# Optimization experiments

Hardware: AMD Instinct MI355X
Metric: run time of the kernel (lower is better)

## Reference

```python
import jax, jax.numpy as jnp
import numpy as np

DIM = 1024
H = 16
HD = DIM // H
EPS_DENOM = 1e-6
EPS_LN = 1e-5


def setup_inputs() -> dict:
    key = jax.random.key(0)
    ks = jax.random.split(key, 8)
    B, N = 4, 4096
    s = 1.0 / np.sqrt(DIM)
    return {
        "x": jax.random.normal(ks[0], (B, N, DIM), dtype=jnp.float32),
        "Wq": jax.random.normal(ks[1], (DIM, DIM), dtype=jnp.float32) * s,
        "bq": jnp.zeros((DIM,), dtype=jnp.float32),
        "Wk": jax.random.normal(ks[2], (DIM, DIM), dtype=jnp.float32) * s,
        "bk": jnp.zeros((DIM,), dtype=jnp.float32),
        "Wv": jax.random.normal(ks[3], (DIM, DIM), dtype=jnp.float32) * s,
        "bv": jnp.zeros((DIM,), dtype=jnp.float32),
        "gamma": jnp.ones((DIM,), dtype=jnp.float32),
        "beta": jnp.zeros((DIM,), dtype=jnp.float32),
    }


def reference(x, Wq, bq, Wk, bk, Wv, bv, gamma, beta):
    B, N, C = x.shape
    # projections; torch Linear applies x @ W.T + b
    q = (x @ Wq.T + bq).reshape(B, N, H, HD)
    k = (x @ Wk.T + bk).reshape(B, N, H, HD)
    v = (x @ Wv.T + bv).reshape(B, N, H, HD)
    q = jax.nn.relu(q)
    k = jax.nn.relu(k)
    kv = jnp.einsum('bnhd,bnhp->bhdp', k, v)         # (B,H,D,D)
    k_sum = k.sum(axis=1)                             # (B,H,D)
    denom = jnp.einsum('bnhd,bhd->bnh', q, k_sum)
    denom = jnp.maximum(denom, EPS_DENOM)[..., None]  # (B,N,H,1)
    ctx = jnp.einsum('bnhd,bhdp->bnhp', q, kv)        # (B,N,H,D)
    out = (ctx / denom).reshape(B, N, C)
    y = out + x
    mu = y.mean(axis=-1, keepdims=True)
    var = y.var(axis=-1, keepdims=True)
    return (y - mu) / jnp.sqrt(var + EPS_LN) * gamma + beta
```

## Files before the change

kernel.cpp:

```cpp
#include <hip/hip_runtime.h>
#include <hip/hip_bf16.h>
#include <stdint.h>

#define DIM 1024
#define HEADS 16
#define HD 64
#define BB 4
#define NN 4096
#define NTOK (BB*NN)

typedef __bf16 bf16;
typedef __bf16 bf16x8 __attribute__((ext_vector_type(8)));
typedef float  f32x4  __attribute__((ext_vector_type(4)));
typedef unsigned short u16x8 __attribute__((ext_vector_type(8)));
typedef unsigned short u16x4 __attribute__((ext_vector_type(4)));

__device__ __forceinline__ float bf2f(unsigned short u) {
    union { unsigned int i; float f; } x; x.i = ((unsigned int)u) << 16; return x.f;
}

__device__ __forceinline__ u16x8 cvt8(f32x4 a, f32x4 b) {
    union { bf16 h[8]; u16x8 u; } r;
    #pragma unroll
    for (int i = 0; i < 4; ++i) { r.h[i] = (bf16)a[i]; r.h[4 + i] = (bf16)b[i]; }
    return r.u;
}

__device__ __forceinline__ u16x8 load8(const void* base, size_t elem, bool isbf) {
    if (isbf) return *(const u16x8*)((const unsigned short*)base + elem);
    const float* p = (const float*)base + elem;
    return cvt8(*(const f32x4*)p, *(const f32x4*)(p + 4));
}

__device__ __forceinline__ void async_copy16(const void* g, void* l) {
    __builtin_amdgcn_global_load_lds(
        (const __attribute__((address_space(1))) void*)g,
        (__attribute__((address_space(3))) void*)l,
        16, 0, 0);
}

__global__ __launch_bounds__(256) void convert_all(
    const void* __restrict__ X,
    const void* __restrict__ Wq, const void* __restrict__ Wk,
    const void* __restrict__ Wv, const uint32_t* __restrict__ det,
    u16x8* __restrict__ Xb, u16x8* __restrict__ Wb)
{
    const bool isbf = (*det == 0x3F803F80u);
    size_t e = ((size_t)blockIdx.x * 256 + threadIdx.x) * 8;
    if (e < 16777216ull) {
        Xb[e >> 3] = load8(X, e, isbf);
    } else {
        size_t r = e - 16777216ull;
        int w = (int)(r >> 20);
        const void* src = (w == 0) ? Wq : (w == 1) ? Wk : Wv;
        Wb[r >> 3] = load8(src, r & 1048575ull, isbf);
    }
}


#define MFMA_Q(Q) do {                                                        \
    _Pragma("unroll")                                                         \
    for (int kb_ = 0; kb_ < 2; ++kb_) {                                       \
        _Pragma("unroll")                                                     \
        for (int i_ = 0; i_ < 2; ++i_) {                                      \
            _Pragma("unroll")                                                 \
            for (int j_ = 0; j_ < 4; ++j_)                                    \
                acc[Q][i_][j_] = __builtin_amdgcn_mfma_f32_16x16x32_bf16(     \
                    afr[i_][kb_], bfrag[j_][kb_], acc[Q][i_][j_], 0, 0, 0);   \
        }                                                                     \
    }                                                                         \
} while (0)

#define PHASE(BUF, Q, DOB, STAGE_STMT, VM_STMT) do {                          \
    bf16x8 afr[2][2];                                                         \
    if (DOB) loadB(BUF);                                                      \
    loadA(BUF, Q, afr);                                                       \
    STAGE_STMT;                                                               \
    VM_STMT;                                                                  \
    __builtin_amdgcn_s_barrier();                                             \
    asm volatile("s_waitcnt lgkmcnt(0)" ::: "memory");                        \
    __builtin_amdgcn_s_setprio(1);                                            \
    MFMA_Q(Q);                                                                \
    __builtin_amdgcn_s_setprio(0);                                            \
    __builtin_amdgcn_s_barrier();                                             \
} while (0)

__global__ __launch_bounds__(512, 2) void qkv_gemm_8ph(
    const bf16* __restrict__ Xb, const bf16* __restrict__ Wb,
    const void* __restrict__ bq, const void* __restrict__ bk,
    const void* __restrict__ bv, const uint32_t* __restrict__ det,
    bf16* __restrict__ outQKV)
{
    extern __shared__ char lds[];

    const bool isbf = (*det == 0x3F803F80u);

    const int bid = blockIdx.x;
    const int xcd = bid & 7;
    const int idx = bid >> 3;
    const int mb  = xcd * 8 + (idx & 7);
    const int nb  = idx >> 3;
    const int m0  = mb * 256;
    const int n0  = nb * 256;
    const int z   = n0 >> 10;
    const int ncol0 = n0 & 1023;
    const void* bias = (z == 0) ? bq : (z == 1) ? bk : bv;
    bf16* out = outQKV + (size_t)z * (size_t)NTOK * DIM;

    const int tid  = threadIdx.x;
    const int wid  = tid >> 6;
    const int lane = tid & 63;
    const int lrow = lane & 15;
    const int lkq  = lane >> 4;
    const int wm   = wid >> 2;
    const int wn   = wid & 3;

    auto stageHT = [&](int kt, int which) {
        const int  buf = kt & 1;
        const bool isB = which >= 2;
        const int  gb  = (which & 1) * 8;
        char* base = lds + buf * 65536 + (isB ? 32768 : 0);
        const int k0 = kt * 64;
        #pragma unroll
        for (int t2 = 0; t2 < 2; ++t2) {
            int s   = wid * 2 + t2;
            int g   = gb + (s >> 1);
            int kb  = s & 1;
            int row = g * 16 + lrow;
            int kk  = k0 + kb * 32 + lkq * 8;
            const bf16* gp = isB ? (Wb + (size_t)(n0 + row) * DIM + kk)
                                 : (Xb + (size_t)(m0 + row) * DIM + kk);
            async_copy16(gp, base + (g * 2 + kb) * 1024);
        }
    };

    bf16x8 bfrag[4][2];
    auto loadB = [&](int buf) {
        char* bB = lds + buf * 65536 + 32768;
        #pragma unroll
        for (int j = 0; j < 4; ++j)
            #pragma unroll
            for (int kb = 0; kb < 2; ++kb)
                bfrag[j][kb] = *(const bf16x8*)(
                    bB + ((wn * 4 + j) * 2 + kb) * 1024 + lane * 16);
    };
    auto loadA = [&](int buf, int q, bf16x8 (&afr)[2][2]) {
        char* bA = lds + buf * 65536;
        #pragma unroll
        for (int i = 0; i < 2; ++i)
            #pragma unroll
            for (int kb = 0; kb < 2; ++kb)
                afr[i][kb] = *(const bf16x8*)(
                    bA + ((q * 4 + wm * 2 + i) * 2 + kb) * 1024 + lane * 16);
    };

    f32x4 acc[4][2][4];
    #pragma unroll
    for (int q = 0; q < 4; ++q)
        #pragma unroll
        for (int i = 0; i < 2; ++i)
            #pragma unroll
            for (int j = 0; j < 4; ++j)
                #pragma unroll
                for (int r = 0; r < 4; ++r) acc[q][i][j][r] = 0.f;

    stageHT(0, 0); stageHT(0, 1); stageHT(0, 2); stageHT(0, 3);
    stageHT(1, 0); stageHT(1, 1); stageHT(1, 2);
    asm volatile("s_waitcnt vmcnt(6)" ::: "memory");
    __builtin_amdgcn_s_barrier();

    for (int ip = 0; ip < 8; ++ip) {
        const int  t    = ip * 2;
        const bool more = (ip < 7);
        PHASE(0, 0, true,  { stageHT(t + 1, 3); },              {});
        PHASE(0, 1, false, { if (more) stageHT(t + 2, 2); },    {});
        PHASE(0, 2, false, { if (more) stageHT(t + 2, 0); },    {});
        PHASE(0, 3, false, { if (more) stageHT(t + 2, 3); },
              { if (more) { asm volatile("s_waitcnt vmcnt(6)" ::: "memory"); }
                else      { asm volatile("s_waitcnt vmcnt(0)" ::: "memory"); } });
        PHASE(1, 0, true,  { if (more) stageHT(t + 2, 1); },    {});
        PHASE(1, 1, false, { if (more) stageHT(t + 3, 2); },    {});
        PHASE(1, 2, false, { if (more) stageHT(t + 3, 0); },    {});
        PHASE(1, 3, false, { if (more) stageHT(t + 3, 1); },
              { if (more) { asm volatile("s_waitcnt vmcnt(6)" ::: "memory"); } });
    }

    #pragma unroll
    for (int q = 0; q < 4; ++q) {
        #pragma unroll
        for (int j = 0; j < 4; ++j) {
            int col = ncol0 + wn * 64 + j * 16 + lrow;
            float bvv = isbf ? bf2f(((const unsigned short*)bias)[col])
                             : ((const float*)bias)[col];
            #pragma unroll
            for (int i = 0; i < 2; ++i) {
                #pragma unroll
                for (int r = 0; r < 4; ++r) {
                    int row = q * 64 + wm * 32 + i * 16 + lkq * 4 + r;
                    float v = acc[q][i][j][r] + bvv;
                    if (z < 2) v = v > 0.f ? v : 0.f;
                    out[(size_t)(m0 + row) * DIM + col] = (bf16)v;
                }
            }
        }
    }
}

__global__ __launch_bounds__(256) void qkv_gemm_sync(
    const void* __restrict__ X,
    const void* __restrict__ Wq, const void* __restrict__ bq,
    const void* __restrict__ Wk, const void* __restrict__ bk,
    const void* __restrict__ Wv, const void* __restrict__ bv,
    const uint32_t* __restrict__ det,
    bf16* __restrict__ outQKV)
{
    __shared__ __align__(16) char ldsA[16384];
    __shared__ __align__(16) char ldsB[16384];

    const bool isbf = (*det == 0x3F803F80u);
    const int z = blockIdx.z;
    const void* W    = (z == 0) ? Wq : (z == 1) ? Wk : Wv;
    const void* bias = (z == 0) ? bq : (z == 1) ? bk : bv;
    bf16* out = outQKV + (size_t)z * (size_t)NTOK * DIM;

    const int m0 = blockIdx.y * 128;
    const int n0 = blockIdx.x * 128;
    const int tid  = threadIdx.x;
    const int wave = tid >> 6;
    const int lane = tid & 63;
    const int lrow = lane & 15;
    const int lkq  = lane >> 4;

    f32x4 acc[4][4];
    #pragma unroll
    for (int i = 0; i < 4; ++i)
        #pragma unroll
        for (int j = 0; j < 4; ++j)
            #pragma unroll
            for (int r = 0; r < 4; ++r) acc[i][j][r] = 0.f;

    const int wRowG = (wave >> 1) * 4;
    const int wColG = (wave & 1) * 4;

    const int sr   = tid & 15;
    const int kc   = (tid >> 4) & 7;
    const int half = tid >> 7;

    for (int k0 = 0; k0 < DIM; k0 += 64) {
        u16x8 va[4], vb[4];
        #pragma unroll
        for (int l = 0; l < 4; ++l) {
            int row = l * 32 + sr + 16 * half;
            va[l] = load8(X, (size_t)(m0 + row) * DIM + k0 + kc * 8, isbf);
            vb[l] = load8(W, (size_t)(n0 + row) * DIM + k0 + kc * 8, isbf);
        }
        __syncthreads();
        #pragma unroll
        for (int l = 0; l < 4; ++l) {
            int row = l * 32 + sr + 16 * half;
            int g = row >> 4, kb = kc >> 2;
            int off = ((g * 2 + kb) * 64 + (kc & 3) * 16 + (row & 15)) * 16;
            *(u16x8*)(ldsA + off) = va[l];
            *(u16x8*)(ldsB + off) = vb[l];
        }
        __syncthreads();

        #pragma unroll
        for (int kb = 0; kb < 2; ++kb) {
            bf16x8 a[4], b[4];
            #pragma unroll
            for (int i = 0; i < 4; ++i)
                a[i] = *(const bf16x8*)(ldsA + ((wRowG + i) * 2 + kb) * 1024 + lane * 16);
            #pragma unroll
            for (int j = 0; j < 4; ++j)
                b[j] = *(const bf16x8*)(ldsB + ((wColG + j) * 2 + kb) * 1024 + lane * 16);
            #pragma unroll
            for (int i = 0; i < 4; ++i)
                #pragma unroll
                for (int j = 0; j < 4; ++j)
                    acc[i][j] = __builtin_amdgcn_mfma_f32_16x16x32_bf16(
                        a[i], b[j], acc[i][j], 0, 0, 0);
        }
    }

    #pragma unroll
    for (int j = 0; j < 4; ++j) {
        int col = (wave & 1) * 64 + j * 16 + lrow;
        float bv_ = isbf ? bf2f(((const unsigned short*)bias)[n0 + col])
                         : ((const float*)bias)[n0 + col];
        #pragma unroll
        for (int i = 0; i < 4; ++i) {
            #pragma unroll
            for (int r = 0; r < 4; ++r) {
                int row = (wave >> 1) * 64 + i * 16 + lkq * 4 + r;
                float v = acc[i][j][r] + bv_;
                if (z < 2) v = v > 0.f ? v : 0.f;
                out[(size_t)(m0 + row) * DIM + (n0 + col)] = (bf16)v;
            }
        }
    }
}

__global__ __launch_bounds__(256) void kv_mfma(
    const bf16* __restrict__ K, const bf16* __restrict__ V,
    float* __restrict__ KVT, float* __restrict__ ksum)
{
    __shared__ __align__(16) char Apan[10240];
    __shared__ __align__(16) char Bpan[8192];

    const int bh = blockIdx.x;
    const int b  = bh >> 4, h = bh & 15;
    const int tok0 = blockIdx.y * 512;
    const int t    = threadIdx.x;
    const int w    = t >> 6;
    const int lane = t & 63;

    #pragma unroll
    for (int u = 0; u < 4; ++u) {
        int ug = u * 256 + t;
        unsigned short val = ((((ug & 511) >> 3) & 15) == 0) ? (unsigned short)0x3F80
                                                             : (unsigned short)0;
        *(unsigned short*)(Apan + 8192 + ug * 2) = val;
    }

    const int P   = t & 31;
    const int d0  = (t >> 5) * 8;
    const int n0t = P * 2;

    f32x4 acc[5];
    #pragma unroll
    for (int g = 0; g < 5; ++g)
        #pragma unroll
        for (int r = 0; r < 4; ++r) acc[g][r] = 0.f;

    const size_t gbase = ((size_t)(b * NN + tok0 + n0t)) * DIM + h * HD + d0;
    u16x8 k0 = *(const u16x8*)(K + gbase);
    u16x8 k1 = *(const u16x8*)(K + gbase + DIM);
    u16x8 v0 = *(const u16x8*)(V + gbase);
    u16x8 v1 = *(const u16x8*)(V + gbase + DIM);

    for (int c = 0; c < 8; ++c) {
        __syncthreads();
        #pragma unroll
        for (int j = 0; j < 8; ++j) {
            int d   = d0 + j;
            int off = ((d >> 4) * 2 + (n0t >> 5)) * 1024
                    + (((n0t & 31) >> 3) * 16 + (d & 15)) * 16 + (n0t & 7) * 2;
            *(uint32_t*)(Bpan + off) = (uint32_t)k0[j] | ((uint32_t)k1[j] << 16);
            *(uint32_t*)(Apan + off) = (uint32_t)v0[j] | ((uint32_t)v1[j] << 16);
        }
        if (c < 7) {
            size_t gn = gbase + (size_t)(c + 1) * 64 * DIM;
            k0 = *(const u16x8*)(K + gn);
            k1 = *(const u16x8*)(K + gn + DIM);
            v0 = *(const u16x8*)(V + gn);
            v1 = *(const u16x8*)(V + gn + DIM);
        }
        __syncthreads();
        bf16x8 bfr0 = *(const bf16x8*)(Bpan + (w * 2 + 0) * 1024 + lane * 16);
        bf16x8 bfr1 = *(const bf16x8*)(Bpan + (w * 2 + 1) * 1024 + lane * 16);
        #pragma unroll
        for (int g = 0; g < 5; ++g) {
            bf16x8 a0 = *(const bf16x8*)(Apan + (g * 2 + 0) * 1024 + lane * 16);
            bf16x8 a1 = *(const bf16x8*)(Apan + (g * 2 + 1) * 1024 + lane * 16);
            acc[g] = __builtin_amdgcn_mfma_f32_16x16x32_bf16(a0, bfr0, acc[g], 0, 0, 0);
            acc[g] = __builtin_amdgcn_mfma_f32_16x16x32_bf16(a1, bfr1, acc[g], 0, 0, 0);
        }
    }

    const int d  = w * 16 + (lane & 15);
    const int pr = (lane >> 4) * 4;
    float* kvtb = KVT + (size_t)bh * HD * HD;
    #pragma unroll
    for (int g = 0; g < 4; ++g)
        #pragma unroll
        for (int r = 0; r < 4; ++r)
            atomicAdd(&kvtb[(g * 16 + pr + r) * HD + d], acc[g][r]);
    if (lane < 16)
        atomicAdd(&ksum[bh * HD + d], acc[4][0]);
}

__global__ __launch_bounds__(256) void ctx_gemm(
    const bf16* __restrict__ Q, const float* __restrict__ KVT,
    const float* __restrict__ ksum, bf16* __restrict__ ctxd)
{
    __shared__ __align__(16) char ldsQ[16384];
    __shared__ __align__(16) char ldsKV[8192];
    __shared__ float ksumL[64];
    __shared__ float denomL[128];

    const int mt = blockIdx.x;
    const int h  = blockIdx.y;
    const int b  = blockIdx.z;
    const int bh = b * 16 + h;
    const int tid  = threadIdx.x;
    const int wave = tid >> 6;
    const int lane = tid & 63;
    const int lrow = lane & 15;
    const int lkq  = lane >> 4;
    const int tokbase = b * NN + mt * 128;

    {
        const int sr = tid >> 3;
        const int kc = tid & 7;
        #pragma unroll
        for (int l = 0; l < 4; ++l) {
            int row = l * 32 + sr;
            u16x8 v = *(const u16x8*)(Q + (size_t)(tokbase + row) * DIM
                                        + h * HD + kc * 8);
            int g = row >> 4, kb = kc >> 2;
            int off = ((g * 2 + kb) * 64 + (kc & 3) * 16 + (row & 15)) * 16;
            *(u16x8*)(ldsQ + off) = v;
        }
    }
    const float* kvtb = KVT + (size_t)bh * HD * HD;
    #pragma unroll
    for (int ii = 0; ii < 2; ++ii) {
        int c = ii * 256 + tid;
        int p = c >> 3, dc = c & 7;
        const float* src = kvtb + p * HD + dc * 8;
        f32x4 v0 = *(const f32x4*)(src);
        f32x4 v1 = *(const f32x4*)(src + 4);
        bf16x8 o;
        #pragma unroll
        for (int jj = 0; jj < 4; ++jj) { o[jj] = (bf16)v0[jj]; o[4 + jj] = (bf16)v1[jj]; }
        int gn = p >> 4, kb = dc >> 2, q = dc & 3;
        *(bf16x8*)(ldsKV + (gn * 2 + kb) * 1024 + (q * 16 + (p & 15)) * 16) = o;
    }
    if (tid < 64) ksumL[tid] = ksum[bh * HD + tid];
    __syncthreads();

    f32x4 acc[2][4];
    #pragma unroll
    for (int i = 0; i < 2; ++i)
        #pragma unroll
        for (int j = 0; j < 4; ++j)
            #pragma unroll
            for (int r = 0; r < 4; ++r) acc[i][j][r] = 0.f;

    #pragma unroll
    for (int kb = 0; kb < 2; ++kb) {
        bf16x8 a[2], bfr[4];
        #pragma unroll
        for (int i = 0; i < 2; ++i)
            a[i] = *(const bf16x8*)(ldsQ + ((wave * 2 + i) * 2 + kb) * 1024 + lane * 16);
        #pragma unroll
        for (int j = 0; j < 4; ++j)
            bfr[j] = *(const bf16x8*)(ldsKV + (j * 2 + kb) * 1024 + lane * 16);
        #pragma unroll
        for (int i = 0; i < 2; ++i)
            #pragma unroll
            for (int j = 0; j < 4; ++j)
                acc[i][j] = __builtin_amdgcn_mfma_f32_16x16x32_bf16(
                    a[i], bfr[j], acc[i][j], 0, 0, 0);
    }

    if (tid < 128) {
        int tok = tid;
        float dot = 0.f;
        #pragma unroll
        for (int kb = 0; kb < 2; ++kb)
            #pragma unroll
            for (int q = 0; q < 4; ++q) {
                bf16x8 qv = *(const bf16x8*)(ldsQ + ((tok >> 4) * 2 + kb) * 1024
                                             + (q * 16 + (tok & 15)) * 16);
                #pragma unroll
                for (int jj = 0; jj < 8; ++jj)
                    dot += (float)qv[jj] * ksumL[kb * 32 + q * 8 + jj];
            }
        denomL[tok] = fmaxf(dot, 1e-6f);
    }
    __syncthreads();

    bf16* outb = ctxd + (size_t)tokbase * DIM + h * HD;
    #pragma unroll
    for (int i = 0; i < 2; ++i)
        #pragma unroll
        for (int j = 0; j < 4; ++j)
            #pragma unroll
            for (int r = 0; r < 4; ++r) {
                int row = wave * 32 + i * 16 + lkq * 4 + r;
                int p   = j * 16 + lrow;
                float v = acc[i][j][r] / denomL[row];
                outb[(size_t)row * DIM + p] = (bf16)v;
            }
}

__global__ __launch_bounds__(256) void ln_kernel(
    const void* __restrict__ Xext, const bf16* __restrict__ Xb, int use_xb,
    const bf16* __restrict__ ctxd,
    const void* __restrict__ gamma, const void* __restrict__ beta,
    const uint32_t* __restrict__ det,
    void* __restrict__ out)
{
    const bool isbf = (*det == 0x3F803F80u);
    const int tok  = blockIdx.x * 4 + (threadIdx.x >> 6);
    const int lane = threadIdx.x & 63;
    const size_t rowbase = (size_t)tok * DIM;

    float y[16];
    float s1 = 0.f, s2 = 0.f;
    #pragma unroll
    for (int q = 0; q < 4; ++q) {
        int e = q * 256 + lane * 4;
        float xv[4];
        if (use_xb) {
            u16x4 xu = *(const u16x4*)(Xb + rowbase + e);
            #pragma unroll
            for (int i = 0; i < 4; ++i) xv[i] = bf2f(xu[i]);
        } else if (isbf) {
            u16x4 xu = *(const u16x4*)((const unsigned short*)Xext + rowbase + e);
            #pragma unroll
            for (int i = 0; i < 4; ++i) xv[i] = bf2f(xu[i]);
        } else {
            f32x4 xf = *(const f32x4*)((const float*)Xext + rowbase + e);
            #pragma unroll
            for (int i = 0; i < 4; ++i) xv[i] = xf[i];
        }
        u16x4 cu = *(const u16x4*)(ctxd + rowbase + e);
        #pragma unroll
        for (int i = 0; i < 4; ++i) {
            float v = xv[i] + bf2f(cu[i]);
            y[q * 4 + i] = v;
            s1 += v;
            s2 += v * v;
        }
    }
    #pragma unroll
    for (int off = 32; off > 0; off >>= 1) {
        s1 += __shfl_xor(s1, off, 64);
        s2 += __shfl_xor(s2, off, 64);
    }
    const float mu = s1 * (1.0f / DIM);
    const float rs = rsqrtf(s2 * (1.0f / DIM) - mu * mu + 1e-5f);

    #pragma unroll
    for (int q = 0; q < 4; ++q) {
        int e = q * 256 + lane * 4;
        float g[4], bb[4];
        if (isbf) {
            u16x4 gu = *(const u16x4*)((const unsigned short*)gamma + e);
            u16x4 bu = *(const u16x4*)((const unsigned short*)beta + e);
            #pragma unroll
            for (int i = 0; i < 4; ++i) { g[i] = bf2f(gu[i]); bb[i] = bf2f(bu[i]); }
        } else {
            f32x4 gf = *(const f32x4*)((const float*)gamma + e);
            f32x4 bf = *(const f32x4*)((const float*)beta + e);
            #pragma unroll
            for (int i = 0; i < 4; ++i) { g[i] = gf[i]; bb[i] = bf[i]; }
        }
        if (isbf) {
            union { bf16 h[4]; u16x4 u; } o;
            #pragma unroll
            for (int i = 0; i < 4; ++i)
                o.h[i] = (bf16)((y[q * 4 + i] - mu) * rs * g[i] + bb[i]);
            *(u16x4*)((unsigned short*)out + rowbase + e) = o.u;
        } else {
            f32x4 o;
            #pragma unroll
            for (int i = 0; i < 4; ++i)
                o[i] = (y[q * 4 + i] - mu) * rs * g[i] + bb[i];
            *(f32x4*)((float*)out + rowbase + e) = o;
        }
    }
}

extern "C" void kernel_launch(void* const* d_in, const int* in_sizes, int n_in,
                              void* d_out, int out_size, void* d_ws, size_t ws_size,
                              hipStream_t stream)
{
    const void* x     = d_in[0];
    const void* Wq    = d_in[1];
    const void* bq    = d_in[2];
    const void* Wk    = d_in[3];
    const void* bk    = d_in[4];
    const void* Wv    = d_in[5];
    const void* bv    = d_in[6];
    const void* gamma = d_in[7];
    const void* beta  = d_in[8];
    const uint32_t* det = (const uint32_t*)gamma;

    char* ws = (char*)d_ws;
    const size_t QKV_BYTES  = 100663296ull;
    const size_t FULL_NEED  = 33554432ull + 6291456ull + QKV_BYTES + 1048576ull + 16384ull;
    const bool full = (ws_size >= FULL_NEED);

    bf16 *Qw, *Xb = nullptr, *Wb = nullptr;
    float *KVT, *ksum;
    if (full) {
        Xb   = (bf16*)ws;
        Wb   = (bf16*)(ws + 33554432ull);
        Qw   = (bf16*)(ws + 39845888ull);
        KVT  = (float*)(ws + 39845888ull + QKV_BYTES);
        ksum = (float*)(ws + 39845888ull + QKV_BYTES + 1048576ull);
    } else {
        Qw   = (bf16*)ws;
        KVT  = (float*)(ws + QKV_BYTES);
        ksum = (float*)(ws + QKV_BYTES + 1048576ull);
    }
    bf16* Kw   = Qw + (size_t)NTOK * DIM;
    bf16* Vw   = Kw + (size_t)NTOK * DIM;
    bf16* ctxd = Kw;

    hipMemsetAsync(KVT, 0, 1048576 + 16384, stream);

    if (full) {
        static int attr_done = 0;
        if (!attr_done) {
            hipFuncSetAttribute(reinterpret_cast<const void*>(qkv_gemm_8ph),
                                hipFuncAttributeMaxDynamicSharedMemorySize, 131072);
            attr_done = 1;
        }
        convert_all<<<9728, 256, 0, stream>>>(x, Wq, Wk, Wv, det, (u16x8*)Xb, (u16x8*)Wb);
        qkv_gemm_8ph<<<768, 512, 131072, stream>>>(Xb, Wb, bq, bk, bv, det, Qw);
    } else {
        qkv_gemm_sync<<<dim3(8, 128, 3), 256, 0, stream>>>(x, Wq, bq, Wk, bk, Wv, bv, det, Qw);
    }

    kv_mfma<<<dim3(64, 8), 256, 0, stream>>>(Kw, Vw, KVT, ksum);

    ctx_gemm<<<dim3(32, HEADS, BB), 256, 0, stream>>>(Qw, KVT, ksum, ctxd);

    ln_kernel<<<NTOK / 4, 256, 0, stream>>>(x, Xb, full ? 1 : 0, ctxd, gamma, beta, det, d_out);
}
```

Before: 307.9 us.

## Fuse ctx GEMM with LayerNorm via LDS-resident ctx rows, fold memset into convert

Replaces the separate ctx_gemm and ln_kernel with one ctx_ln kernel. Each block computes attention context for 64 tokens across all 16 heads into a large LDS buffer, then applies residual and LayerNorm directly. The ksum denominator is computed as an extra MFMA tile, and zeroing of KVT/ksum is folded into the conversion kernel instead of a memset. This removes the global ctx round-trip and a launch, at the cost of far fewer blocks (256, one per CU due to ~150KB LDS) and a serial per-head loop with barriers.

Measured after the change: 334.0 us. 1.08x slower.

```diff
diff --git a/kernel.cpp b/kernel.cpp
--- a/kernel.cpp
+++ b/kernel.cpp
@@ -19,6 +19,10 @@
     union { unsigned int i; float f; } x; x.i = ((unsigned int)u) << 16; return x.f;
 }
 
+__device__ __forceinline__ unsigned short f2bf_u16(float f) {
+    union { bf16 h; unsigned short u; } r; r.h = (bf16)f; return r.u;
+}
+
 __device__ __forceinline__ u16x8 cvt8(f32x4 a, f32x4 b) {
     union { bf16 h[8]; u16x8 u; } r;
     #pragma unroll
@@ -43,17 +47,21 @@
     const void* __restrict__ X,
     const void* __restrict__ Wq, const void* __restrict__ Wk,
     const void* __restrict__ Wv, const uint32_t* __restrict__ det,
-    u16x8* __restrict__ Xb, u16x8* __restrict__ Wb)
+    u16x8* __restrict__ Xb, u16x8* __restrict__ Wb,
+    f32x4* __restrict__ zreg)
 {
     const bool isbf = (*det == 0x3F803F80u);
     size_t e = ((size_t)blockIdx.x * 256 + threadIdx.x) * 8;
     if (e < 16777216ull) {
         Xb[e >> 3] = load8(X, e, isbf);
-    } else {
+    } else if (e < 19922944ull) {
         size_t r = e - 16777216ull;
         int w = (int)(r >> 20);
         const void* src = (w == 0) ? Wq : (w == 1) ? Wk : Wv;
         Wb[r >> 3] = load8(src, r & 1048575ull, isbf);
+    } else {
+        size_t zi = (e - 19922944ull) >> 3;
+        zreg[zi] = f32x4{0.f, 0.f, 0.f, 0.f};
     }
 }
 
@@ -380,187 +388,176 @@
         atomicAdd(&ksum[bh * HD + d], acc[4][0]);
 }
 
-__global__ __launch_bounds__(256) void ctx_gemm(
+#define CTXL_STRIDE 1044
+__global__ __launch_bounds__(256) void ctx_ln(
     const bf16* __restrict__ Q, const float* __restrict__ KVT,
-    const float* __restrict__ ksum, bf16* __restrict__ ctxd)
-{
-    __shared__ __align__(16) char ldsQ[16384];
-    __shared__ __align__(16) char ldsKV[8192];
-    __shared__ float ksumL[64];
-    __shared__ float denomL[128];
-
-    const int mt = blockIdx.x;
-    const int h  = blockIdx.y;
-    const int b  = blockIdx.z;
-    const int bh = b * 16 + h;
-    const int tid  = threadIdx.x;
-    const int wave = tid >> 6;
-    const int lane = tid & 63;
-    const int lrow = lane & 15;
-    const int lkq  = lane >> 4;
-    const int tokbase = b * NN + mt * 128;
-
-    {
-        const int sr = tid >> 3;
-        const int kc = tid & 7;
-        #pragma unroll
-        for (int l = 0; l < 4; ++l) {
-            int row = l * 32 + sr;
-            u16x8 v = *(const u16x8*)(Q + (size_t)(tokbase + row) * DIM
-                                        + h * HD + kc * 8);
-            int g = row >> 4, kb = kc >> 2;
-            int off = ((g * 2 + kb) * 64 + (kc & 3) * 16 + (row & 15)) * 16;
-            *(u16x8*)(ldsQ + off) = v;
-        }
-    }
-    const float* kvtb = KVT + (size_t)bh * HD * HD;
-    #pragma unroll
-    for (int ii = 0; ii < 2; ++ii) {
-        int c = ii * 256 + tid;
-        int p = c >> 3, dc = c & 7;
-        const float* src = kvtb + p * HD + dc * 8;
-        f32x4 v0 = *(const f32x4*)(src);
-        f32x4 v1 = *(const f32x4*)(src + 4);
-        bf16x8 o;
-        #pragma unroll
-        for (int jj = 0; jj < 4; ++jj) { o[jj] = (bf16)v0[jj]; o[4 + jj] = (bf16)v1[jj]; }
-        int gn = p >> 4, kb = dc >> 2, q = dc & 3;
-        *(bf16x8*)(ldsKV + (gn * 2 + kb) * 1024 + (q * 16 + (p & 15)) * 16) = o;
-    }
-    if (tid < 64) ksumL[tid] = ksum[bh * HD + tid];
-    __syncthreads();
-
-    f32x4 acc[2][4];
-    #pragma unroll
-    for (int i = 0; i < 2; ++i)
-        #pragma unroll
-        for (int j = 0; j < 4; ++j)
-            #pragma unroll
-            for (int r = 0; r < 4; ++r) acc[i][j][r] = 0.f;
-
-    #pragma unroll
-    for (int kb = 0; kb < 2; ++kb) {
-        bf16x8 a[2], bfr[4];
-        #pragma unroll
-        for (int i = 0; i < 2; ++i)
-            a[i] = *(const bf16x8*)(ldsQ + ((wave * 2 + i) * 2 + kb) * 1024 + lane * 16);
-        #pragma unroll
-        for (int j = 0; j < 4; ++j)
-            bfr[j] = *(const bf16x8*)(ldsKV + (j * 2 + kb) * 1024 + lane * 16);
-        #pragma unroll
-        for (int i = 0; i < 2; ++i)
-            #pragma unroll
-            for (int j = 0; j < 4; ++j)
-                acc[i][j] = __builtin_amdgcn_mfma_f32_16x16x32_bf16(
-                    a[i], bfr[j], acc[i][j], 0, 0, 0);
-    }
-
-    if (tid < 128) {
-        int tok = tid;
-        float dot = 0.f;
-        #pragma unroll
-        for (int kb = 0; kb < 2; ++kb)
-            #pragma unroll
-            for (int q = 0; q < 4; ++q) {
-                bf16x8 qv = *(const bf16x8*)(ldsQ + ((tok >> 4) * 2 + kb) * 1024
-                                             + (q * 16 + (tok & 15)) * 16);
-                #pragma unroll
-                for (int jj = 0; jj < 8; ++jj)
-                    dot += (float)qv[jj] * ksumL[kb * 32 + q * 8 + jj];
-            }
-        denomL[tok] = fmaxf(dot, 1e-6f);
-    }
-    __syncthreads();
-
-    bf16* outb = ctxd + (size_t)tokbase * DIM + h * HD;
-    #pragma unroll
-    for (int i = 0; i < 2; ++i)
-        #pragma unroll
-        for (int j = 0; j < 4; ++j)
-            #pragma unroll
-            for (int r = 0; r < 4; ++r) {
-                int row = wave * 32 + i * 16 + lkq * 4 + r;
-                int p   = j * 16 + lrow;
-                float v = acc[i][j][r] / denomL[row];
-                outb[(size_t)row * DIM + p] = (bf16)v;
-            }
-}
-
-__global__ __launch_bounds__(256) void ln_kernel(
+    const float* __restrict__ ksum,
     const void* __restrict__ Xext, const bf16* __restrict__ Xb, int use_xb,
-    const bf16* __restrict__ ctxd,
     const void* __restrict__ gamma, const void* __restrict__ beta,
     const uint32_t* __restrict__ det,
     void* __restrict__ out)
 {
+    extern __shared__ char lds[];
+    unsigned short* ctxL = (unsigned short*)lds;
+    char* ldsQ  = lds + 133632;
+    char* ldsKV = lds + 141824;
+
     const bool isbf = (*det == 0x3F803F80u);
-    const int tok  = blockIdx.x * 4 + (threadIdx.x >> 6);
-    const int lane = threadIdx.x & 63;
-    const size_t rowbase = (size_t)tok * DIM;
-
-    float y[16];
-    float s1 = 0.f, s2 = 0.f;
-    #pragma unroll
-    for (int q = 0; q < 4; ++q) {
-        int e = q * 256 + lane * 4;
-        float xv[4];
-        if (use_xb) {
-            u16x4 xu = *(const u16x4*)(Xb + rowbase + e);
-            #pragma unroll
-            for (int i = 0; i < 4; ++i) xv[i] = bf2f(xu[i]);
-        } else if (isbf) {
-            u16x4 xu = *(const u16x4*)((const unsigned short*)Xext + rowbase + e);
-            #pragma unroll
-            for (int i = 0; i < 4; ++i) xv[i] = bf2f(xu[i]);
-        } else {
-            f32x4 xf = *(const f32x4*)((const float*)Xext + rowbase + e);
-            #pragma unroll
-            for (int i = 0; i < 4; ++i) xv[i] = xf[i];
-        }
-        u16x4 cu = *(const u16x4*)(ctxd + rowbase + e);
-        #pragma unroll
-        for (int i = 0; i < 4; ++i) {
-            float v = xv[i] + bf2f(cu[i]);
-            y[q * 4 + i] = v;
-            s1 += v;
-            s2 += v * v;
-        }
-    }
-    #pragma unroll
-    for (int off = 32; off > 0; off >>= 1) {
-        s1 += __shfl_xor(s1, off, 64);
-        s2 += __shfl_xor(s2, off, 64);
-    }
-    const float mu = s1 * (1.0f / DIM);
-    const float rs = rsqrtf(s2 * (1.0f / DIM) - mu * mu + 1e-5f);
-
-    #pragma unroll
-    for (int q = 0; q < 4; ++q) {
-        int e = q * 256 + lane * 4;
-        float g[4], bb[4];
-        if (isbf) {
-            u16x4 gu = *(const u16x4*)((const unsigned short*)gamma + e);
-            u16x4 bu = *(const u16x4*)((const unsigned short*)beta + e);
-            #pragma unroll
-            for (int i = 0; i < 4; ++i) { g[i] = bf2f(gu[i]); bb[i] = bf2f(bu[i]); }
-        } else {
-            f32x4 gf = *(const f32x4*)((const float*)gamma + e);
-            f32x4 bf = *(const f32x4*)((const float*)beta + e);
-            #pragma unroll
-            for (int i = 0; i < 4; ++i) { g[i] = gf[i]; bb[i] = bf[i]; }
-        }
-        if (isbf) {
-            union { bf16 h[4]; u16x4 u; } o;
-            #pragma unroll
-            for (int i = 0; i < 4; ++i)
-                o.h[i] = (bf16)((y[q * 4 + i] - mu) * rs * g[i] + bb[i]);
-            *(u16x4*)((unsigned short*)out + rowbase + e) = o.u;
-        } else {
-            f32x4 o;
-            #pragma unroll
-            for (int i = 0; i < 4; ++i)
-                o[i] = (y[q * 4 + i] - mu) * rs * g[i] + bb[i];
-            *(f32x4*)((float*)out + rowbase + e) = o;
+    const int blk = blockIdx.x;
+    const int tokbase = blk * 64;
+    const int b = blk >> 6;
+    const int tid  = threadIdx.x;
+    const int w    = tid >> 6;
+    const int lane = tid & 63;
+    const int lkq  = lane >> 4;
+    const int lcol = lane & 15;
+
+    for (int h = 0; h < 16; ++h) {
+        const int bh = b * 16 + h;
+        #pragma unroll
+        for (int l = 0; l < 2; ++l) {
+            int row = l * 32 + (tid >> 3);
+            int kc  = tid & 7;
+            u16x8 v = *(const u16x8*)(Q + (size_t)(tokbase + row) * DIM
+                                        + h * HD + kc * 8);
+            int off = ((row >> 4) * 2 + (kc >> 2)) * 1024
+                    + ((kc & 3) * 16 + (row & 15)) * 16;
+            *(u16x8*)(ldsQ + off) = v;
+        }
+        const float* kvtb = KVT + (size_t)bh * HD * HD;
+        #pragma unroll
+        for (int ii = 0; ii < 2; ++ii) {
+            int c = ii * 256 + tid;
+            int p = c >> 3, dc = c & 7;
+            const float* src = kvtb + p * HD + dc * 8;
+            f32x4 v0 = *(const f32x4*)(src);
+            f32x4 v1 = *(const f32x4*)(src + 4);
+            bf16x8 o;
+            #pragma unroll
+            for (int jj = 0; jj < 4; ++jj) { o[jj] = (bf16)v0[jj]; o[4 + jj] = (bf16)v1[jj]; }
+            int gn = p >> 4, kb = dc >> 2, q = dc & 3;
+            *(bf16x8*)(ldsKV + (gn * 2 + kb) * 1024 + (q * 16 + (p & 15)) * 16) = o;
+        }
+        {
+            const float* ks = ksum + bh * HD;
+            #pragma unroll
+            for (int i = 0; i < 2; ++i) {
+                int u = i * 256 + tid;
+                int kb = u >> 8, rem = u & 255;
+                int q = rem >> 6, prow = (rem >> 2) & 15, wslot = rem & 3;
+                uint32_t val = 0;
+                if (prow == 0) {
+                    int k = kb * 32 + q * 8 + wslot * 2;
+                    val = (uint32_t)f2bf_u16(ks[k])
+                        | ((uint32_t)f2bf_u16(ks[k + 1]) << 16);
+                }
+                *(uint32_t*)(ldsKV + (8 + kb) * 1024 + (q * 16 + prow) * 16
+                             + wslot * 4) = val;
+            }
+        }
+        __syncthreads();
+        bf16x8 a[2], bfr[5][2];
+        #pragma unroll
+        for (int kb = 0; kb < 2; ++kb)
+            a[kb] = *(const bf16x8*)(ldsQ + (w * 2 + kb) * 1024 + lane * 16);
+        #pragma unroll
+        for (int g = 0; g < 5; ++g)
+            #pragma unroll
+            for (int kb = 0; kb < 2; ++kb)
+                bfr[g][kb] = *(const bf16x8*)(ldsKV + (g * 2 + kb) * 1024 + lane * 16);
+        __syncthreads();
+        f32x4 acc[5];
+        #pragma unroll
+        for (int g = 0; g < 5; ++g)
+            #pragma unroll
+            for (int r = 0; r < 4; ++r) acc[g][r] = 0.f;
+        #pragma unroll
+        for (int g = 0; g < 5; ++g)
+            #pragma unroll
+            for (int kb = 0; kb < 2; ++kb)
+                acc[g] = __builtin_amdgcn_mfma_f32_16x16x32_bf16(
+                    a[kb], bfr[g][kb], acc[g], 0, 0, 0);
+        #pragma unroll
+        for (int r = 0; r < 4; ++r) {
+            float dv = __shfl(acc[4][r], lane & 48, 64);
+            float inv = 1.0f / fmaxf(dv, 1e-6f);
+            int tokl = w * 16 + lkq * 4 + r;
+            #pragma unroll
+            for (int g = 0; g < 4; ++g)
+                ctxL[tokl * CTXL_STRIDE + h * 64 + g * 16 + lcol] =
+                    f2bf_u16(acc[g][r] * inv);
+        }
+    }
+    __syncthreads();
+
+    for (int tt = 0; tt < 16; ++tt) {
+        const int tokl = w * 16 + tt;
+        const size_t rowbase = (size_t)(tokbase + tokl) * DIM;
+
+        float y[16];
+        float s1 = 0.f, s2 = 0.f;
+        #pragma unroll
+        for (int q = 0; q < 4; ++q) {
+            int e = q * 256 + lane * 4;
+            float xv[4];
+            if (use_xb) {
+                u16x4 xu = *(const u16x4*)(Xb + rowbase + e);
+                #pragma unroll
+                for (int i = 0; i < 4; ++i) xv[i] = bf2f(xu[i]);
+            } else if (isbf) {
+                u16x4 xu = *(const u16x4*)((const unsigned short*)Xext + rowbase + e);
+                #pragma unroll
+                for (int i = 0; i < 4; ++i) xv[i] = bf2f(xu[i]);
+            } else {
+                f32x4 xf = *(const f32x4*)((const float*)Xext + rowbase + e);
+                #pragma unroll
+                for (int i = 0; i < 4; ++i) xv[i] = xf[i];
+            }
+            u16x4 cu = *(const u16x4*)(ctxL + tokl * CTXL_STRIDE + e);
+            #pragma unroll
+            for (int i = 0; i < 4; ++i) {
+                float v = xv[i] + bf2f(cu[i]);
+                y[q * 4 + i] = v;
+                s1 += v;
+                s2 += v * v;
+            }
+        }
+        #pragma unroll
+        for (int off = 32; off > 0; off >>= 1) {
+            s1 += __shfl_xor(s1, off, 64);
+            s2 += __shfl_xor(s2, off, 64);
+        }
+        const float mu = s1 * (1.0f / DIM);
+        const float rs = rsqrtf(s2 * (1.0f / DIM) - mu * mu + 1e-5f);
+
+        #pragma unroll
+        for (int q = 0; q < 4; ++q) {
+            int e = q * 256 + lane * 4;
+            float g[4], bb[4];
+            if (isbf) {
+                u16x4 gu = *(const u16x4*)((const unsigned short*)gamma + e);
+                u16x4 bu = *(const u16x4*)((const unsigned short*)beta + e);
+                #pragma unroll
+                for (int i = 0; i < 4; ++i) { g[i] = bf2f(gu[i]); bb[i] = bf2f(bu[i]); }
+            } else {
+                f32x4 gf = *(const f32x4*)((const float*)gamma + e);
+                f32x4 bf = *(const f32x4*)((const float*)beta + e);
+                #pragma unroll
+                for (int i = 0; i < 4; ++i) { g[i] = gf[i]; bb[i] = bf[i]; }
+            }
+            if (isbf) {
+                union { bf16 h2[4]; u16x4 u; } o;
+                #pragma unroll
+                for (int i = 0; i < 4; ++i)
+                    o.h2[i] = (bf16)((y[q * 4 + i] - mu) * rs * g[i] + bb[i]);
+                *(u16x4*)((unsigned short*)out + rowbase + e) = o.u;
+            } else {
+                f32x4 o;
+                #pragma unroll
+                for (int i = 0; i < 4; ++i)
+                    o[i] = (y[q * 4 + i] - mu) * rs * g[i] + bb[i];
+                *(f32x4*)((float*)out + rowbase + e) = o;
+            }
         }
     }
 }
@@ -598,28 +595,29 @@
         KVT  = (float*)(ws + QKV_BYTES);
         ksum = (float*)(ws + QKV_BYTES + 1048576ull);
     }
-    bf16* Kw   = Qw + (size_t)NTOK * DIM;
-    bf16* Vw   = Kw + (size_t)NTOK * DIM;
-    bf16* ctxd = Kw;
-
-    hipMemsetAsync(KVT, 0, 1048576 + 16384, stream);
+    bf16* Kw = Qw + (size_t)NTOK * DIM;
+    bf16* Vw = Kw + (size_t)NTOK * DIM;
+
+    static int attr_done = 0;
+    if (!attr_done) {
+        hipFuncSetAttribute(reinterpret_cast<const void*>(qkv_gemm_8ph),
+                            hipFuncAttributeMaxDynamicSharedMemorySize, 131072);
+        hipFuncSetAttribute(reinterpret_cast<const void*>(ctx_ln),
+                            hipFuncAttributeMaxDynamicSharedMemorySize, 152064);
+        attr_done = 1;
+    }
 
     if (full) {
-        static int attr_done = 0;
-        if (!attr_done) {
-            hipFuncSetAttribute(reinterpret_cast<const void*>(qkv_gemm_8ph),
-                                hipFuncAttributeMaxDynamicSharedMemorySize, 131072);
-            attr_done = 1;
-        }
-        convert_all<<<9728, 256, 0, stream>>>(x, Wq, Wk, Wv, det, (u16x8*)Xb, (u16x8*)Wb);
+        convert_all<<<9988, 256, 0, stream>>>(x, Wq, Wk, Wv, det,
+                                              (u16x8*)Xb, (u16x8*)Wb, (f32x4*)KVT);
         qkv_gemm_8ph<<<768, 512, 131072, stream>>>(Xb, Wb, bq, bk, bv, det, Qw);
     } else {
+        hipMemsetAsync(KVT, 0, 1048576 + 16384, stream);
         qkv_gemm_sync<<<dim3(8, 128, 3), 256, 0, stream>>>(x, Wq, bq, Wk, bk, Wv, bv, det, Qw);
     }
 
     kv_mfma<<<dim3(64, 8), 256, 0, stream>>>(Kw, Vw, KVT, ksum);
 
-    ctx_gemm<<<dim3(32, HEADS, BB), 256, 0, stream>>>(Qw, KVT, ksum, ctxd);
-
-    ln_kernel<<<NTOK / 4, 256, 0, stream>>>(x, Xb, full ? 1 : 0, ctxd, gamma, beta, det, d_out);
-}
+    ctx_ln<<<256, 256, 152064, stream>>>(Qw, KVT, ksum, x, Xb, full ? 1 : 0,
+                                         gamma, beta, det, d_out);
+}
```
